# Performance work log

Measured on AMD Instinct MI355X. Metric: run time of the kernel, lower is better.

Reference implementation:

```python
import jax, jax.numpy as jnp
import numpy as np


def setup_inputs() -> dict:
    key = jax.random.key(0)
    k_x, k_q, k_k, k_v = jax.random.split(key, 4)
    seq_len, d_in, d_out = 4096, 1024, 1024
    x = jax.random.normal(k_x, (seq_len, d_in), dtype=jnp.float32)
    # torch nn.Linear weights are [d_out, d_in]; applied as x @ W.T
    scale = 1.0 / np.sqrt(d_in)
    Wq = jax.random.uniform(k_q, (d_out, d_in), jnp.float32, -scale, scale)
    Wk = jax.random.uniform(k_k, (d_out, d_in), jnp.float32, -scale, scale)
    Wv = jax.random.uniform(k_v, (d_out, d_in), jnp.float32, -scale, scale)
    return {"x": x, "Wq": Wq, "Wk": Wk, "Wv": Wv}


def reference(x, Wq, Wk, Wv):
    # x: [S, d_in]; Wq/Wk/Wv: [d_out, d_in]
    queries = x @ Wq.T          # [S, d_out]
    keys = x @ Wk.T             # [S, d_out]
    values = x @ Wv.T           # [S, d_out]
    d_k = keys.shape[-1]
    attn_scores = queries @ keys.T                      # [S, S]
    attn_weights = jax.nn.softmax(attn_scores / jnp.sqrt(jnp.float32(d_k)), axis=-1)
    S = attn_scores.shape[0]
    tril = jnp.tril(jnp.ones((S, S), dtype=attn_weights.dtype))
    masked = tril * attn_weights
    masked_norm = masked / jnp.sum(masked, axis=-1, keepdims=True)
    context_vec = masked_norm @ values                  # [S, d_out]
    return context_vec
```

## Files before the change

### kernel.cpp

```cpp
#include <hip/hip_runtime.h>
#include <hip/hip_bf16.h>


typedef __bf16 bf16_t;
typedef __bf16 bf16x4v __attribute__((ext_vector_type(4)));
typedef __bf16 bf16x8 __attribute__((ext_vector_type(8)));
typedef float f32x4 __attribute__((ext_vector_type(4)));
typedef unsigned char u8;
typedef long long i64_t;

#define AS1 __attribute__((address_space(1)))
#define AS3 __attribute__((address_space(3)))
#define WAIT_VMCNT(N) asm volatile("s_waitcnt vmcnt(" #N ")" ::: "memory")
#define BARRIER_RAW() asm volatile("s_barrier" ::: "memory")

__device__ __forceinline__ void async_copy16(const void* g, void* l) {
    __builtin_amdgcn_global_load_lds((AS1 void*)(g), (AS3 void*)(l), 16, 0, 0);
}

__device__ __forceinline__ u8 f32_to_fp8(float v) {
    return (u8)(__builtin_amdgcn_cvt_pk_fp8_f32(v, v, 0, false) & 0xff);
}

__device__ __forceinline__ void store_conv(float* p, float v) { *p = v; }
__device__ __forceinline__ void store_conv(bf16_t* p, float v) { *p = (bf16_t)v; }
__device__ __forceinline__ void store_conv(u8* p, float v) { *p = f32_to_fp8(v); }

__device__ __forceinline__ float sum32(const float* p) {
    const f32x4* v = (const f32x4*)p;
    float s = 0.f;
#pragma unroll
    for (int u = 0; u < 8; ++u) {
        f32x4 a = v[u];
        s += a[0] + a[1] + a[2] + a[3];
    }
    return s;
}

template <int EPI, typename OutT>
__device__ __forceinline__ void gemm_tile_bf16(const bf16_t* __restrict__ A, int lda,
                                               const bf16_t* __restrict__ B, int ldb,
                                               OutT* __restrict__ C, int ldc,
                                               int kb0, int kb1, float alpha,
                                               char* __restrict__ smem,
                                               const float* __restrict__ inv) {
    constexpr int BK = 64;
    bf16_t* As = (bf16_t*)smem;
    bf16_t* Bs = (bf16_t*)(smem + 32768);
    const int tid = threadIdx.x;
    const int lane = tid & 63, wave = tid >> 6;
    const int wm = wave >> 1, wn = wave & 1;
    const int q = lane >> 4, l16 = lane & 15;

    f32x4 acc[4][4] = {};

    const bf16_t* aSrc[4];
    const bf16_t* bSrc[4];
    int ldsOff[4];
#pragma unroll
    for (int it = 0; it < 4; ++it) {
        int c = it * 256 + tid;
        int r = c >> 3, b = c & 7;
        int sb = b ^ (r & 7);
        aSrc[it] = A + (size_t)r * lda + sb * 8;
        bSrc[it] = B + (size_t)r * ldb + sb * 8;
        ldsOff[it] = c * 8;
    }

    {
        const int k0 = kb0 * BK;
#pragma unroll
        for (int it = 0; it < 4; ++it) async_copy16(aSrc[it] + k0, &As[ldsOff[it]]);
#pragma unroll
        for (int it = 0; it < 4; ++it) async_copy16(bSrc[it] + k0, &Bs[ldsOff[it]]);
    }

    int cur = 0;
    for (int kb = kb0; kb < kb1; ++kb) {
        if (kb + 1 < kb1) {
            const int k0 = (kb + 1) * BK;
            const int boff = (cur ^ 1) * 8192;
#pragma unroll
            for (int it = 0; it < 4; ++it) async_copy16(aSrc[it] + k0, &As[boff + ldsOff[it]]);
#pragma unroll
            for (int it = 0; it < 4; ++it) async_copy16(bSrc[it] + k0, &Bs[boff + ldsOff[it]]);
            WAIT_VMCNT(8);
        } else {
            WAIT_VMCNT(0);
        }
        __builtin_amdgcn_sched_barrier(0);
        BARRIER_RAW();
        const bf16_t* Ab = As + cur * 8192;
        const bf16_t* Bb = Bs + cur * 8192;
        __builtin_amdgcn_s_setprio(1);
#pragma unroll
        for (int k2 = 0; k2 < 2; ++k2) {
            bf16x8 af[4], bfr[4];
#pragma unroll
            for (int mt = 0; mt < 4; ++mt) {
                int m = wm * 64 + mt * 16 + l16;
                int blk = (k2 * 4 + q) ^ (m & 7);
                af[mt] = *(const bf16x8*)&Ab[m * BK + blk * 8];
            }
#pragma unroll
            for (int nt = 0; nt < 4; ++nt) {
                int nn = wn * 64 + nt * 16 + l16;
                int blk = (k2 * 4 + q) ^ (nn & 7);
                bfr[nt] = *(const bf16x8*)&Bb[nn * BK + blk * 8];
            }
#pragma unroll
            for (int mt = 0; mt < 4; ++mt)
#pragma unroll
                for (int nt = 0; nt < 4; ++nt)
                    acc[mt][nt] = __builtin_amdgcn_mfma_f32_16x16x32_bf16(
                        af[mt], bfr[nt], acc[mt][nt], 0, 0, 0);
        }
        __builtin_amdgcn_s_setprio(0);
        BARRIER_RAW();
        cur ^= 1;
    }

    constexpr int S = (int)sizeof(OutT);
    constexpr int RB = 128 * S;
    const int row0 = wm * 64, col0 = wn * 64;
#pragma unroll
    for (int mt = 0; mt < 4; ++mt)
#pragma unroll
        for (int nt = 0; nt < 4; ++nt)
#pragma unroll
            for (int r = 0; r < 4; ++r) {
                int lr = row0 + mt * 16 + q * 4 + r;
                int lc = col0 + nt * 16 + l16;
                float v = acc[mt][nt][r];
                v = (EPI == 2) ? v * inv[lr] : v * alpha;
                int cb = (lc * S) >> 4;
                int sw = cb ^ ((lr >> 2) & 7);
                store_conv((OutT*)(smem + lr * RB + (sw << 4) + ((lc * S) & 15)), v);
            }
    __syncthreads();
#pragma unroll
    for (int p = 0; p < 4 * S; ++p) {
        int g = p * 4096 + tid * 16;
        int r = g / RB;
        int wb = g & (RB - 1);
        int sc = (wb >> 4) ^ ((r >> 2) & 7);
        f32x4 val = *(const f32x4*)(smem + r * RB + (sc << 4));
        *(f32x4*)((char*)C + (size_t)r * ((size_t)ldc * S) + wb) = val;
    }
}

__device__ __forceinline__ void scores_tile_fp8(const u8* __restrict__ A, int lda,
                                                const u8* __restrict__ B, int ldb,
                                                bf16_t* __restrict__ C, int ldc,
                                                float alpha, char* __restrict__ smem,
                                                float* __restrict__ partial,
                                                int gr0, int gc0) {
    u8* As = (u8*)smem;
    u8* Bs = (u8*)(smem + 32768);
    const int tid = threadIdx.x;
    const int lane = tid & 63, wave = tid >> 6;
    const int wm = wave >> 1, wn = wave & 1;
    const int q = lane >> 4, l16 = lane & 15;

    f32x4 acc[4][4] = {};

    const u8* aSrc[4];
    const u8* bSrc[4];
    int ldsOff[4];
#pragma unroll
    for (int it = 0; it < 4; ++it) {
        int c = it * 256 + tid;
        int r = c >> 3, b = c & 7;
        int sb = b ^ (r & 7);
        aSrc[it] = A + (size_t)r * lda + sb * 16;
        bSrc[it] = B + (size_t)r * ldb + sb * 16;
        ldsOff[it] = c * 16;
    }

    {
#pragma unroll
        for (int it = 0; it < 4; ++it) async_copy16(aSrc[it], &As[ldsOff[it]]);
#pragma unroll
        for (int it = 0; it < 4; ++it) async_copy16(bSrc[it], &Bs[ldsOff[it]]);
    }

    int cur = 0;
    for (int kb = 0; kb < 8; ++kb) {
        if (kb < 7) {
            const int k0 = (kb + 1) * 128;
            const int boff = (cur ^ 1) * 16384;
#pragma unroll
            for (int it = 0; it < 4; ++it) async_copy16(aSrc[it] + k0, &As[boff + ldsOff[it]]);
#pragma unroll
            for (int it = 0; it < 4; ++it) async_copy16(bSrc[it] + k0, &Bs[boff + ldsOff[it]]);
            WAIT_VMCNT(8);
        } else {
            WAIT_VMCNT(0);
        }
        __builtin_amdgcn_sched_barrier(0);
        BARRIER_RAW();
        const u8* Ab = As + cur * 16384;
        const u8* Bb = Bs + cur * 16384;
        __builtin_amdgcn_s_setprio(1);
#pragma unroll
        for (int k2 = 0; k2 < 4; ++k2) {
            i64_t af[4], bfr[4];
            const int cb = 2 * k2 + (q >> 1), co = (q & 1) * 8;
#pragma unroll
            for (int mt = 0; mt < 4; ++mt) {
                int m = wm * 64 + mt * 16 + l16;
                af[mt] = *(const i64_t*)&Ab[m * 128 + ((cb ^ (m & 7)) << 4) + co];
            }
#pragma unroll
            for (int nt = 0; nt < 4; ++nt) {
                int nn = wn * 64 + nt * 16 + l16;
                bfr[nt] = *(const i64_t*)&Bb[nn * 128 + ((cb ^ (nn & 7)) << 4) + co];
            }
#pragma unroll
            for (int mt = 0; mt < 4; ++mt)
#pragma unroll
                for (int nt = 0; nt < 4; ++nt)
                    acc[mt][nt] = __builtin_amdgcn_mfma_f32_16x16x32_fp8_fp8(
                        af[mt], bfr[nt], acc[mt][nt], 0, 0, 0);
        }
        __builtin_amdgcn_s_setprio(0);
        BARRIER_RAW();
        cur ^= 1;
    }

    float* sred = (float*)(smem + 32768);
    const int row0 = wm * 64, col0 = wn * 64;
    float esum[4][4];
#pragma unroll
    for (int mt = 0; mt < 4; ++mt)
#pragma unroll
        for (int r = 0; r < 4; ++r) esum[mt][r] = 0.f;
#pragma unroll
    for (int mt = 0; mt < 4; ++mt)
#pragma unroll
        for (int nt = 0; nt < 4; ++nt)
#pragma unroll
            for (int r = 0; r < 4; ++r) {
                int lr = row0 + mt * 16 + q * 4 + r;
                int lc = col0 + nt * 16 + l16;
                float pe = (gc0 + lc > gr0 + lr) ? 0.f : __expf(acc[mt][nt][r] * alpha);
                esum[mt][r] += pe;
                int sw = (lc >> 3) ^ ((lr >> 2) & 7);
                *(bf16_t*)(smem + lr * 256 + (sw << 4) + ((lc * 2) & 15)) = (bf16_t)pe;
            }
#pragma unroll
    for (int mt = 0; mt < 4; ++mt)
#pragma unroll
        for (int r = 0; r < 4; ++r) {
#pragma unroll
            for (int off = 1; off < 16; off <<= 1)
                esum[mt][r] += __shfl_xor(esum[mt][r], off, 64);
            if (l16 == 0) sred[(row0 + mt * 16 + q * 4 + r) * 2 + wn] = esum[mt][r];
        }
    __syncthreads();
#pragma unroll
    for (int p = 0; p < 8; ++p) {
        int g = p * 4096 + tid * 16;
        int r = g >> 8;
        int wb = g & 255;
        int sc = (wb >> 4) ^ ((r >> 2) & 7);
        f32x4 val = *(const f32x4*)(smem + r * 256 + (sc << 4));
        *(f32x4*)((char*)C + (size_t)r * ((size_t)ldc * 2) + wb) = val;
    }
    if (tid < 128) partial[(size_t)tid * 32] = sred[tid * 2] + sred[tid * 2 + 1];
}

__global__ __launch_bounds__(256) void k_qkv(const bf16_t* __restrict__ xb,
                                             const bf16_t* __restrict__ wqk,
                                             u8* __restrict__ qk) {
    __shared__ __attribute__((aligned(16))) char smem[65536];
    int b = blockIdx.x;
    int bm = b & 31, bn = b >> 5;
    gemm_tile_bf16<0, u8>(xb + (size_t)bm * 128 * 1024, 1024,
                          wqk + (size_t)bn * 128 * 1024, 1024,
                          qk + (size_t)bm * 128 * 2048 + bn * 128, 2048,
                          0, 16, 1.f, smem, nullptr);
}

__global__ __launch_bounds__(256) void k_sv(const bf16_t* __restrict__ xb,
                                            const bf16_t* __restrict__ wvb,
                                            const u8* __restrict__ qk,
                                            bf16_t* __restrict__ vt,
                                            bf16_t* __restrict__ P,
                                            float* __restrict__ rowsum_part) {
    __shared__ __attribute__((aligned(16))) char smem[65536];
    int b = blockIdx.x;
    if (b < 256) {
        int bm = b & 7, bn = b >> 3;
        gemm_tile_bf16<0, bf16_t>(wvb + (size_t)bm * 128 * 1024, 1024,
                                  xb + (size_t)bn * 128 * 1024, 1024,
                                  vt + (size_t)bm * 128 * 4096 + bn * 128, 4096,
                                  0, 16, 1.f, smem, nullptr);
        return;
    }
    int t = b - 256;
    int bm = (int)((sqrtf(8.f * (float)t + 1.f) - 1.f) * 0.5f);
    while (bm * (bm + 1) / 2 > t) --bm;
    while ((bm + 1) * (bm + 2) / 2 <= t) ++bm;
    int bn = t - bm * (bm + 1) / 2;
    scores_tile_fp8(qk + (size_t)bm * 128 * 2048, 2048,
                    qk + 1024 + (size_t)bn * 128 * 2048, 2048,
                    P + (size_t)bm * 128 * 4096 + bn * 128, 4096,
                    0.03125f, smem,
                    rowsum_part + (size_t)bm * 128 * 32 + bn,
                    bm * 128, bn * 128);
    if (bn == bm) {
        float* rp = rowsum_part + (size_t)bm * 128 * 32;
        int tid = threadIdx.x;
        for (int r = tid >> 4; r < 128; r += 16)
            for (int u = bm + 1 + (tid & 15); u < 32; u += 16)
                rp[r * 32 + u] = 0.f;
    }
}

__global__ __launch_bounds__(256) void k_pv(const bf16_t* __restrict__ P,
                                            const bf16_t* __restrict__ vt,
                                            const float* __restrict__ rowsum_part,
                                            float* __restrict__ out,
                                            float* __restrict__ partials) {
    __shared__ __attribute__((aligned(16))) char smem[65536];
    __shared__ float sInv[128];
    int b = blockIdx.x;
    int bn = b & 7, g = b >> 3;
    int bm, s, ns;
    if (g < 8)       { bm = g;                 s = 0;            ns = 1; }
    else if (g < 24) { bm = 8 + (g - 8) / 2;   s = (g - 8) % 2;  ns = 2; }
    else if (g < 48) { bm = 16 + (g - 24) / 3; s = (g - 24) % 3; ns = 3; }
    else             { bm = 24 + (g - 48) / 4; s = (g - 48) % 4; ns = 4; }
    int nk = 2 * (bm + 1);
    int kb0 = s * nk / ns;
    int kb1 = (s + 1) * nk / ns;

    const bf16_t* A = P + (size_t)bm * 128 * 4096;
    const bf16_t* B = vt + (size_t)bn * 128 * 4096;
    if (ns == 1) {
        int tid = threadIdx.x;
        if (tid < 128)
            sInv[tid] = 1.f / sum32(rowsum_part + (size_t)(bm * 128 + tid) * 32);
        gemm_tile_bf16<2, float>(A, 4096, B, 4096,
                                 out + (size_t)bm * 128 * 1024 + bn * 128, 1024,
                                 kb0, kb1, 1.f, smem, sInv);
    } else {
        int cum = (bm < 16) ? (bm - 8) * 2
                : (bm < 24) ? 16 + (bm - 16) * 3
                            : 40 + (bm - 24) * 4;
        gemm_tile_bf16<0, float>(A, 4096, B, 4096,
                                 partials + ((size_t)(cum + s) * 8 + bn) * 16384, 128,
                                 kb0, kb1, 1.f, smem, nullptr);
    }
}

__global__ __launch_bounds__(256) void k_reduce(const float* __restrict__ partials,
                                                const float* __restrict__ rowsum_part,
                                                float* __restrict__ out) {
    int b = blockIdx.x;
    int t = b % 192, p = b / 192;
    int bm = t % 24 + 8, bn = t / 24;
    int ns = (bm < 16) ? 2 : (bm < 24) ? 3 : 4;
    int cum = (bm < 16) ? (bm - 8) * 2
            : (bm < 24) ? 16 + (bm - 16) * 3
                        : 40 + (bm - 24) * 4;
    __shared__ float sInv[8];
    int tid = threadIdx.x;
    if (tid < 8) {
        int row = bm * 128 + p * 8 + tid;
        sInv[tid] = 1.f / sum32(rowsum_part + (size_t)row * 32);
    }
    __syncthreads();

    int idx = p * 1024 + tid * 4;
    int lr = idx >> 7, lc = idx & 127;
    float sx = 0.f, sy = 0.f, sz = 0.f, sw = 0.f;
    for (int u = 0; u < ns; ++u) {
        const float4 v = *(const float4*)(partials + ((size_t)(cum + u) * 8 + bn) * 16384 + idx);
        sx += v.x; sy += v.y; sz += v.z; sw += v.w;
    }
    float inv = sInv[lr - p * 8];
    float4 o = {sx * inv, sy * inv, sz * inv, sw * inv};
    *(float4*)(out + (size_t)(bm * 128 + lr) * 1024 + bn * 128 + lc) = o;
}

__global__ __launch_bounds__(256) void cast_to_bf16(const float* __restrict__ x,
                                                    const float* __restrict__ Wq,
                                                    const float* __restrict__ Wk,
                                                    const float* __restrict__ Wv,
                                                    bf16_t* __restrict__ xb,
                                                    bf16_t* __restrict__ wqk,
                                                    bf16_t* __restrict__ wv) {
    const int NX = (4096 * 1024) / 4;
    const int NW = (1024 * 1024) / 4;
    int idx = blockIdx.x * 256 + threadIdx.x;
    const float* src;
    bf16_t* dst;
    int off;
    if (idx < NX) {
        src = x; dst = xb; off = idx;
    } else if (idx < NX + NW) {
        src = Wq; dst = wqk; off = idx - NX;
    } else if (idx < NX + 2 * NW) {
        src = Wk; dst = wqk + (size_t)NW * 4; off = idx - NX - NW;
    } else {
        src = Wv; dst = wv; off = idx - NX - 2 * NW;
    }
    float4 f = ((const float4*)src)[off];
    bf16x4v o;
    o.x = (bf16_t)f.x; o.y = (bf16_t)f.y; o.z = (bf16_t)f.z; o.w = (bf16_t)f.w;
    *(bf16x4v*)(dst + (size_t)off * 4) = o;
}

extern "C" void kernel_launch(void* const* d_in, const int* in_sizes, int n_in,
                              void* d_out, int out_size, void* d_ws, size_t ws_size,
                              hipStream_t stream) {
    (void)in_sizes; (void)n_in; (void)out_size; (void)ws_size;
    const float* x  = (const float*)d_in[0];
    const float* Wq = (const float*)d_in[1];
    const float* Wk = (const float*)d_in[2];
    const float* Wv = (const float*)d_in[3];
    float* out = (float*)d_out;

    char* ws = (char*)d_ws;
    bf16_t* xb   = (bf16_t*)(ws + (size_t)0);
    bf16_t* wqk  = (bf16_t*)(ws + ((size_t)8 << 20));
    bf16_t* wvb  = (bf16_t*)(ws + ((size_t)12 << 20));
    u8*     qk   = (u8*)(ws + ((size_t)14 << 20));
    bf16_t* vt   = (bf16_t*)(ws + ((size_t)22 << 20));
    bf16_t* P    = (bf16_t*)(ws + ((size_t)30 << 20));
    float* rowsp = (float*)(ws + ((size_t)62 << 20));
    float* parts = (float*)(ws + ((size_t)64 << 20));

    cast_to_bf16<<<7168, 256, 0, stream>>>(x, Wq, Wk, Wv, xb, wqk, wvb);

    k_qkv<<<512, 256, 0, stream>>>(xb, wqk, qk);

    k_sv<<<784, 256, 0, stream>>>(xb, wvb, qk, vt, P, rowsp);

    k_pv<<<640, 256, 0, stream>>>(P, vt, rowsp, out, parts);
    k_reduce<<<3072, 256, 0, stream>>>(parts, rowsp, out);
}
```

Measured before the change: 181.2 us.

## Split scores into dedicated 256x128 fp8 kernel and merge V projection into QK GEMM

Moves the V-projection GEMM out of the scores launch and into the QK projection launch, so Q/K/V projections run as one 768-block grid. The causal score tiles get their own kernel with 512-thread blocks, 256x128 tiles and 96KB shared memory. It uses a restructured double-buffered loop that interleaves fragment reads, async prefetch and MFMA phases. Larger tiles raise operand reuse per LDS load but give fewer blocks (272) and one block per CU, which may hurt load balance on the triangular work.

```diff
diff --git a/kernel.cpp b/kernel.cpp
--- a/kernel.cpp
+++ b/kernel.cpp
@@ -149,172 +149,225 @@
     }
 }
 
-__device__ __forceinline__ void scores_tile_fp8(const u8* __restrict__ A, int lda,
-                                                const u8* __restrict__ B, int ldb,
-                                                bf16_t* __restrict__ C, int ldc,
-                                                float alpha, char* __restrict__ smem,
-                                                float* __restrict__ partial,
-                                                int gr0, int gc0) {
-    u8* As = (u8*)smem;
-    u8* Bs = (u8*)(smem + 32768);
+__device__ __forceinline__ void read_afrags(i64_t af[4][2], const u8* Ab,
+                                            int wm, int mh, int k2h,
+                                            int l16, int q) {
+#pragma unroll
+    for (int mt = 0; mt < 4; ++mt)
+#pragma unroll
+        for (int kk = 0; kk < 2; ++kk) {
+            int m = wm * 128 + (mh * 4 + mt) * 16 + l16;
+            int k2 = k2h * 2 + kk;
+            int cb = 2 * k2 + (q >> 1), co = (q & 1) * 8;
+            af[mt][kk] = *(const i64_t*)&Ab[m * 128 + ((cb ^ (m & 7)) << 4) + co];
+        }
+}
+__device__ __forceinline__ void read_bfrags(i64_t bf[2][2], const u8* Bb,
+                                            int wn, int k2h, int l16, int q) {
+#pragma unroll
+    for (int nt = 0; nt < 2; ++nt)
+#pragma unroll
+        for (int kk = 0; kk < 2; ++kk) {
+            int nn = wn * 32 + nt * 16 + l16;
+            int k2 = k2h * 2 + kk;
+            int cb = 2 * k2 + (q >> 1), co = (q & 1) * 8;
+            bf[nt][kk] = *(const i64_t*)&Bb[nn * 128 + ((cb ^ (nn & 7)) << 4) + co];
+        }
+}
+
+__global__ __launch_bounds__(512, 1) void k_scores(const u8* __restrict__ qk,
+                                                   bf16_t* __restrict__ P,
+                                                   float* __restrict__ rowsum_part) {
+    __shared__ __attribute__((aligned(16))) char smem[98304];
+    int t = blockIdx.x;
+    int bm = (int)(sqrtf((float)t + 0.25f) - 0.5f);
+    while (bm * (bm + 1) > t) --bm;
+    while ((bm + 1) * (bm + 2) <= t) ++bm;
+    int bn = t - bm * (bm + 1);
+    const u8* A = qk + (size_t)bm * 256 * 2048;
+    const u8* B = qk + 1024 + (size_t)bn * 128 * 2048;
+    const int gr0 = bm * 256, gc0 = bn * 128;
+    bf16_t* Cc = P + (size_t)bm * 256 * 4096 + bn * 128;
+    float* partial = rowsum_part + (size_t)bm * 256 * 32 + bn;
+
     const int tid = threadIdx.x;
     const int lane = tid & 63, wave = tid >> 6;
-    const int wm = wave >> 1, wn = wave & 1;
+    const int wm = wave >> 2, wn = wave & 3;
     const int q = lane >> 4, l16 = lane & 15;
 
-    f32x4 acc[4][4] = {};
-
-    const u8* aSrc[4];
-    const u8* bSrc[4];
-    int ldsOff[4];
-#pragma unroll
-    for (int it = 0; it < 4; ++it) {
-        int c = it * 256 + tid;
-        int r = c >> 3, b = c & 7;
-        int sb = b ^ (r & 7);
-        aSrc[it] = A + (size_t)r * lda + sb * 16;
-        bSrc[it] = B + (size_t)r * ldb + sb * 16;
-        ldsOff[it] = c * 16;
-    }
-
-    {
-#pragma unroll
-        for (int it = 0; it < 4; ++it) async_copy16(aSrc[it], &As[ldsOff[it]]);
-#pragma unroll
-        for (int it = 0; it < 4; ++it) async_copy16(bSrc[it], &Bs[ldsOff[it]]);
-    }
-
-    int cur = 0;
-    for (int kb = 0; kb < 8; ++kb) {
-        if (kb < 7) {
-            const int k0 = (kb + 1) * 128;
-            const int boff = (cur ^ 1) * 16384;
-#pragma unroll
-            for (int it = 0; it < 4; ++it) async_copy16(aSrc[it] + k0, &As[boff + ldsOff[it]]);
-#pragma unroll
-            for (int it = 0; it < 4; ++it) async_copy16(bSrc[it] + k0, &Bs[boff + ldsOff[it]]);
-            WAIT_VMCNT(8);
-        } else {
-            WAIT_VMCNT(0);
-        }
-        __builtin_amdgcn_sched_barrier(0);
-        BARRIER_RAW();
-        const u8* Ab = As + cur * 16384;
-        const u8* Bb = Bs + cur * 16384;
+    f32x4 acc[8][2] = {};
+
+    const u8* aSrc[4]; int aOff[4];
+    const u8* bSrc[2]; int bOff[2];
+#pragma unroll
+    for (int pp = 0; pp < 4; ++pp) {
+        int g16 = pp * 512 + tid, r = g16 >> 3, b = g16 & 7, sb = b ^ (r & 7);
+        aSrc[pp] = A + (size_t)r * 2048 + sb * 16;
+        aOff[pp] = g16 * 16;
+    }
+#pragma unroll
+    for (int pp = 0; pp < 2; ++pp) {
+        int g16 = pp * 512 + tid, r = g16 >> 3, b = g16 & 7, sb = b ^ (r & 7);
+        bSrc[pp] = B + (size_t)r * 2048 + sb * 16;
+        bOff[pp] = g16 * 16;
+    }
+
+#pragma unroll
+    for (int pp = 0; pp < 4; ++pp) async_copy16(aSrc[pp], smem + aOff[pp]);
+#pragma unroll
+    for (int pp = 0; pp < 2; ++pp) async_copy16(bSrc[pp], smem + 32768 + bOff[pp]);
+    WAIT_VMCNT(0);
+    BARRIER_RAW();
+
+    for (int kt = 0; kt < 8; ++kt) {
+        const char* bufb = smem + (kt & 1) * 49152;
+        char* bufn = smem + ((kt & 1) ^ 1) * 49152;
+        const u8* Ab = (const u8*)bufb;
+        const u8* Bb = (const u8*)(bufb + 32768);
+        const int k0n = (kt + 1) * 128;
+        i64_t af[4][2], bf[2][2];
+
+        read_afrags(af, Ab, wm, 0, 0, l16, q);
+        read_bfrags(bf, Bb, wn, 0, l16, q);
+        if (kt < 7) {
+            async_copy16(aSrc[0] + k0n, bufn + aOff[0]);
+            async_copy16(aSrc[1] + k0n, bufn + aOff[1]);
+            async_copy16(bSrc[0] + k0n, bufn + 32768 + bOff[0]);
+        }
+        BARRIER_RAW();
         __builtin_amdgcn_s_setprio(1);
 #pragma unroll
-        for (int k2 = 0; k2 < 4; ++k2) {
-            i64_t af[4], bfr[4];
-            const int cb = 2 * k2 + (q >> 1), co = (q & 1) * 8;
-#pragma unroll
-            for (int mt = 0; mt < 4; ++mt) {
-                int m = wm * 64 + mt * 16 + l16;
-                af[mt] = *(const i64_t*)&Ab[m * 128 + ((cb ^ (m & 7)) << 4) + co];
-            }
-#pragma unroll
-            for (int nt = 0; nt < 4; ++nt) {
-                int nn = wn * 64 + nt * 16 + l16;
-                bfr[nt] = *(const i64_t*)&Bb[nn * 128 + ((cb ^ (nn & 7)) << 4) + co];
-            }
-#pragma unroll
-            for (int mt = 0; mt < 4; ++mt)
-#pragma unroll
-                for (int nt = 0; nt < 4; ++nt)
+        for (int mt = 0; mt < 4; ++mt)
+#pragma unroll
+            for (int nt = 0; nt < 2; ++nt)
+#pragma unroll
+                for (int kk = 0; kk < 2; ++kk)
                     acc[mt][nt] = __builtin_amdgcn_mfma_f32_16x16x32_fp8_fp8(
-                        af[mt], bfr[nt], acc[mt][nt], 0, 0, 0);
-        }
+                        af[mt][kk], bf[nt][kk], acc[mt][nt], 0, 0, 0);
         __builtin_amdgcn_s_setprio(0);
         BARRIER_RAW();
-        cur ^= 1;
-    }
-
-    float* sred = (float*)(smem + 32768);
-    const int row0 = wm * 64, col0 = wn * 64;
-    float esum[4][4];
-#pragma unroll
-    for (int mt = 0; mt < 4; ++mt)
+
+        read_afrags(af, Ab, wm, 1, 0, l16, q);
+        if (kt < 7) {
+            async_copy16(aSrc[2] + k0n, bufn + aOff[2]);
+            async_copy16(aSrc[3] + k0n, bufn + aOff[3]);
+            async_copy16(bSrc[1] + k0n, bufn + 32768 + bOff[1]);
+        }
+        BARRIER_RAW();
+        __builtin_amdgcn_s_setprio(1);
+#pragma unroll
+        for (int mt = 0; mt < 4; ++mt)
+#pragma unroll
+            for (int nt = 0; nt < 2; ++nt)
+#pragma unroll
+                for (int kk = 0; kk < 2; ++kk)
+                    acc[4 + mt][nt] = __builtin_amdgcn_mfma_f32_16x16x32_fp8_fp8(
+                        af[mt][kk], bf[nt][kk], acc[4 + mt][nt], 0, 0, 0);
+        __builtin_amdgcn_s_setprio(0);
+        BARRIER_RAW();
+
+        read_afrags(af, Ab, wm, 0, 1, l16, q);
+        read_bfrags(bf, Bb, wn, 1, l16, q);
+        BARRIER_RAW();
+        __builtin_amdgcn_s_setprio(1);
+#pragma unroll
+        for (int mt = 0; mt < 4; ++mt)
+#pragma unroll
+            for (int nt = 0; nt < 2; ++nt)
+#pragma unroll
+                for (int kk = 0; kk < 2; ++kk)
+                    acc[mt][nt] = __builtin_amdgcn_mfma_f32_16x16x32_fp8_fp8(
+                        af[mt][kk], bf[nt][kk], acc[mt][nt], 0, 0, 0);
+        __builtin_amdgcn_s_setprio(0);
+        BARRIER_RAW();
+
+        read_afrags(af, Ab, wm, 1, 1, l16, q);
+        BARRIER_RAW();
+        __builtin_amdgcn_s_setprio(1);
+#pragma unroll
+        for (int mt = 0; mt < 4; ++mt)
+#pragma unroll
+            for (int nt = 0; nt < 2; ++nt)
+#pragma unroll
+                for (int kk = 0; kk < 2; ++kk)
+                    acc[4 + mt][nt] = __builtin_amdgcn_mfma_f32_16x16x32_fp8_fp8(
+                        af[mt][kk], bf[nt][kk], acc[4 + mt][nt], 0, 0, 0);
+        __builtin_amdgcn_s_setprio(0);
+        if (kt < 7) WAIT_VMCNT(0);
+        BARRIER_RAW();
+    }
+
+    float* sred = (float*)(smem + 65536);
+    float esum[8][4];
+#pragma unroll
+    for (int mt = 0; mt < 8; ++mt)
 #pragma unroll
         for (int r = 0; r < 4; ++r) esum[mt][r] = 0.f;
 #pragma unroll
-    for (int mt = 0; mt < 4; ++mt)
-#pragma unroll
-        for (int nt = 0; nt < 4; ++nt)
+    for (int mt = 0; mt < 8; ++mt)
+#pragma unroll
+        for (int nt = 0; nt < 2; ++nt)
 #pragma unroll
             for (int r = 0; r < 4; ++r) {
-                int lr = row0 + mt * 16 + q * 4 + r;
-                int lc = col0 + nt * 16 + l16;
-                float pe = (gc0 + lc > gr0 + lr) ? 0.f : __expf(acc[mt][nt][r] * alpha);
+                int lr = wm * 128 + mt * 16 + q * 4 + r;
+                int lc = wn * 32 + nt * 16 + l16;
+                float pe = (gc0 + lc > gr0 + lr) ? 0.f
+                                                 : __expf(acc[mt][nt][r] * 0.03125f);
                 esum[mt][r] += pe;
                 int sw = (lc >> 3) ^ ((lr >> 2) & 7);
                 *(bf16_t*)(smem + lr * 256 + (sw << 4) + ((lc * 2) & 15)) = (bf16_t)pe;
             }
 #pragma unroll
-    for (int mt = 0; mt < 4; ++mt)
+    for (int mt = 0; mt < 8; ++mt)
 #pragma unroll
         for (int r = 0; r < 4; ++r) {
+            float s = esum[mt][r];
 #pragma unroll
             for (int off = 1; off < 16; off <<= 1)
-                esum[mt][r] += __shfl_xor(esum[mt][r], off, 64);
-            if (l16 == 0) sred[(row0 + mt * 16 + q * 4 + r) * 2 + wn] = esum[mt][r];
+                s += __shfl_xor(s, off, 64);
+            if (l16 == 0)
+                sred[(wm * 128 + mt * 16 + q * 4 + r) * 4 + wn] = s;
         }
     __syncthreads();
 #pragma unroll
     for (int p = 0; p < 8; ++p) {
-        int g = p * 4096 + tid * 16;
-        int r = g >> 8;
-        int wb = g & 255;
+        int g = p * 8192 + tid * 16;
+        int r = g >> 8, wb = g & 255;
         int sc = (wb >> 4) ^ ((r >> 2) & 7);
         f32x4 val = *(const f32x4*)(smem + r * 256 + (sc << 4));
-        *(f32x4*)((char*)C + (size_t)r * ((size_t)ldc * 2) + wb) = val;
-    }
-    if (tid < 128) partial[(size_t)tid * 32] = sred[tid * 2] + sred[tid * 2 + 1];
-}
-
-__global__ __launch_bounds__(256) void k_qkv(const bf16_t* __restrict__ xb,
-                                             const bf16_t* __restrict__ wqk,
-                                             u8* __restrict__ qk) {
+        *(f32x4*)((char*)Cc + (size_t)r * 8192 + wb) = val;
+    }
+    if (tid < 256)
+        partial[(size_t)tid * 32] =
+            sred[tid * 4] + sred[tid * 4 + 1] + sred[tid * 4 + 2] + sred[tid * 4 + 3];
+    if (bn == 2 * bm + 1) {
+        float* rp = rowsum_part + (size_t)bm * 256 * 32;
+        for (int r = tid >> 4; r < 256; r += 32)
+            for (int u = 2 * bm + 2 + (tid & 15); u < 32; u += 16)
+                rp[r * 32 + u] = 0.f;
+    }
+}
+
+__global__ __launch_bounds__(256) void k_qkvv(const bf16_t* __restrict__ xb,
+                                              const bf16_t* __restrict__ wqk,
+                                              const bf16_t* __restrict__ wvb,
+                                              u8* __restrict__ qk,
+                                              bf16_t* __restrict__ vt) {
     __shared__ __attribute__((aligned(16))) char smem[65536];
     int b = blockIdx.x;
-    int bm = b & 31, bn = b >> 5;
-    gemm_tile_bf16<0, u8>(xb + (size_t)bm * 128 * 1024, 1024,
-                          wqk + (size_t)bn * 128 * 1024, 1024,
-                          qk + (size_t)bm * 128 * 2048 + bn * 128, 2048,
-                          0, 16, 1.f, smem, nullptr);
-}
-
-__global__ __launch_bounds__(256) void k_sv(const bf16_t* __restrict__ xb,
-                                            const bf16_t* __restrict__ wvb,
-                                            const u8* __restrict__ qk,
-                                            bf16_t* __restrict__ vt,
-                                            bf16_t* __restrict__ P,
-                                            float* __restrict__ rowsum_part) {
-    __shared__ __attribute__((aligned(16))) char smem[65536];
-    int b = blockIdx.x;
-    if (b < 256) {
-        int bm = b & 7, bn = b >> 3;
+    if (b < 512) {
+        int bm = b & 31, bn = b >> 5;
+        gemm_tile_bf16<0, u8>(xb + (size_t)bm * 128 * 1024, 1024,
+                              wqk + (size_t)bn * 128 * 1024, 1024,
+                              qk + (size_t)bm * 128 * 2048 + bn * 128, 2048,
+                              0, 16, 1.f, smem, nullptr);
+    } else {
+        int bb = b - 512;
+        int bm = bb & 7, bn = bb >> 3;
         gemm_tile_bf16<0, bf16_t>(wvb + (size_t)bm * 128 * 1024, 1024,
                                   xb + (size_t)bn * 128 * 1024, 1024,
                                   vt + (size_t)bm * 128 * 4096 + bn * 128, 4096,
                                   0, 16, 1.f, smem, nullptr);
-        return;
-    }
-    int t = b - 256;
-    int bm = (int)((sqrtf(8.f * (float)t + 1.f) - 1.f) * 0.5f);
-    while (bm * (bm + 1) / 2 > t) --bm;
-    while ((bm + 1) * (bm + 2) / 2 <= t) ++bm;
-    int bn = t - bm * (bm + 1) / 2;
-    scores_tile_fp8(qk + (size_t)bm * 128 * 2048, 2048,
-                    qk + 1024 + (size_t)bn * 128 * 2048, 2048,
-                    P + (size_t)bm * 128 * 4096 + bn * 128, 4096,
-                    0.03125f, smem,
-                    rowsum_part + (size_t)bm * 128 * 32 + bn,
-                    bm * 128, bn * 128);
-    if (bn == bm) {
-        float* rp = rowsum_part + (size_t)bm * 128 * 32;
-        int tid = threadIdx.x;
-        for (int r = tid >> 4; r < 128; r += 16)
-            for (int u = bm + 1 + (tid & 15); u < 32; u += 16)
-                rp[r * 32 + u] = 0.f;
     }
 }
 
@@ -435,9 +488,9 @@
 
     cast_to_bf16<<<7168, 256, 0, stream>>>(x, Wq, Wk, Wv, xb, wqk, wvb);
 
-    k_qkv<<<512, 256, 0, stream>>>(xb, wqk, qk);
-
-    k_sv<<<784, 256, 0, stream>>>(xb, wvb, qk, vt, P, rowsp);
+    k_qkvv<<<768, 256, 0, stream>>>(xb, wqk, wvb, qk, vt);
+
+    k_scores<<<272, 512, 0, stream>>>(qk, P, rowsp);
 
     k_pv<<<640, 256, 0, stream>>>(P, vt, rowsp, out, parts);
     k_reduce<<<3072, 256, 0, stream>>>(parts, rowsp, out);
```

Measured after the change: 206.8 us. 14.2% more time.

## Restructure fp8 scores GEMM into 4-stage 64-wide K pipeline with ping-pong phases

Applied to the files above, without the earlier changes.

Replaces the double-buffered 128-wide K loop in the fp8 scores tile with a four-slot ring of 64-wide K chunks, prefetching three chunks ahead. Each K step is split into two phases (top and bottom M halves), with the A and B loads for the next slot interleaved between barriers. The aim is to hide global-to-LDS latency better and overlap LDS reads with MFMA work. It adds more barriers per K step and uses a new LDS swizzle.

```diff
diff --git a/kernel.cpp b/kernel.cpp
--- a/kernel.cpp
+++ b/kernel.cpp
@@ -12,6 +12,7 @@
 #define AS1 __attribute__((address_space(1)))
 #define AS3 __attribute__((address_space(3)))
 #define WAIT_VMCNT(N) asm volatile("s_waitcnt vmcnt(" #N ")" ::: "memory")
+#define WAIT_LGKM0() asm volatile("s_waitcnt lgkmcnt(0)" ::: "memory")
 #define BARRIER_RAW() asm volatile("s_barrier" ::: "memory")
 
 __device__ __forceinline__ void async_copy16(const void* g, void* l) {
@@ -155,8 +156,6 @@
                                                 float alpha, char* __restrict__ smem,
                                                 float* __restrict__ partial,
                                                 int gr0, int gc0) {
-    u8* As = (u8*)smem;
-    u8* Bs = (u8*)(smem + 32768);
     const int tid = threadIdx.x;
     const int lane = tid & 63, wave = tid >> 6;
     const int wm = wave >> 1, wn = wave & 1;
@@ -164,68 +163,102 @@
 
     f32x4 acc[4][4] = {};
 
-    const u8* aSrc[4];
-    const u8* bSrc[4];
-    int ldsOff[4];
-#pragma unroll
-    for (int it = 0; it < 4; ++it) {
-        int c = it * 256 + tid;
-        int r = c >> 3, b = c & 7;
-        int sb = b ^ (r & 7);
-        aSrc[it] = A + (size_t)r * lda + sb * 16;
-        bSrc[it] = B + (size_t)r * ldb + sb * 16;
-        ldsOff[it] = c * 16;
-    }
-
-    {
-#pragma unroll
-        for (int it = 0; it < 4; ++it) async_copy16(aSrc[it], &As[ldsOff[it]]);
-#pragma unroll
-        for (int it = 0; it < 4; ++it) async_copy16(bSrc[it], &Bs[ldsOff[it]]);
-    }
-
-    int cur = 0;
-    for (int kb = 0; kb < 8; ++kb) {
-        if (kb < 7) {
-            const int k0 = (kb + 1) * 128;
-            const int boff = (cur ^ 1) * 16384;
-#pragma unroll
-            for (int it = 0; it < 4; ++it) async_copy16(aSrc[it] + k0, &As[boff + ldsOff[it]]);
-#pragma unroll
-            for (int it = 0; it < 4; ++it) async_copy16(bSrc[it] + k0, &Bs[boff + ldsOff[it]]);
-            WAIT_VMCNT(8);
-        } else {
-            WAIT_VMCNT(0);
+    const u8* aS[2];
+    const u8* bS[2];
+    int lOff[2];
+#pragma unroll
+    for (int p = 0; p < 2; ++p) {
+        int g = p * 256 + tid, r = g >> 2, c = g & 3;
+        int sc = c ^ ((r >> 1) & 3);
+        aS[p] = A + (size_t)r * lda + sc * 16;
+        bS[p] = B + (size_t)r * ldb + sc * 16;
+        lOff[p] = g * 16;
+    }
+
+#pragma unroll
+    for (int h = 0; h < 3; ++h) {
+        char* s = smem + h * 16384;
+        async_copy16(aS[0] + h * 64, s + lOff[0]);
+        async_copy16(aS[1] + h * 64, s + lOff[1]);
+        async_copy16(bS[0] + h * 64, s + 8192 + lOff[0]);
+        async_copy16(bS[1] + h * 64, s + 8192 + lOff[1]);
+    }
+    WAIT_VMCNT(8);
+    __builtin_amdgcn_sched_barrier(0);
+    BARRIER_RAW();
+
+    for (int h = 0; h < 16; ++h) {
+        const u8* Ab = (const u8*)(smem + (h & 3) * 16384);
+        const u8* Bb = Ab + 8192;
+        char* nslot = smem + ((h + 3) & 3) * 16384;
+        const int kn = (h + 3) * 64;
+        i64_t bf[4][2], af[2][2], af2[2][2];
+
+#pragma unroll
+        for (int nt = 0; nt < 4; ++nt)
+#pragma unroll
+            for (int kk = 0; kk < 2; ++kk) {
+                int nn = wn * 64 + nt * 16 + l16;
+                int cb = kk * 2 + (q >> 1);
+                bf[nt][kk] = *(const i64_t*)&Bb[nn * 64 + ((cb ^ ((nn >> 1) & 3)) << 4) + (q & 1) * 8];
+            }
+#pragma unroll
+        for (int mt = 0; mt < 2; ++mt)
+#pragma unroll
+            for (int kk = 0; kk < 2; ++kk) {
+                int m = wm * 64 + mt * 16 + l16;
+                int cb = kk * 2 + (q >> 1);
+                af[mt][kk] = *(const i64_t*)&Ab[m * 64 + ((cb ^ ((m >> 1) & 3)) << 4) + (q & 1) * 8];
+            }
+        if (h <= 12) {
+            async_copy16(aS[0] + kn, nslot + lOff[0]);
+            async_copy16(aS[1] + kn, nslot + lOff[1]);
         }
+        BARRIER_RAW();
+        WAIT_LGKM0();
         __builtin_amdgcn_sched_barrier(0);
-        BARRIER_RAW();
-        const u8* Ab = As + cur * 16384;
-        const u8* Bb = Bs + cur * 16384;
         __builtin_amdgcn_s_setprio(1);
 #pragma unroll
-        for (int k2 = 0; k2 < 4; ++k2) {
-            i64_t af[4], bfr[4];
-            const int cb = 2 * k2 + (q >> 1), co = (q & 1) * 8;
-#pragma unroll
-            for (int mt = 0; mt < 4; ++mt) {
-                int m = wm * 64 + mt * 16 + l16;
-                af[mt] = *(const i64_t*)&Ab[m * 128 + ((cb ^ (m & 7)) << 4) + co];
-            }
-#pragma unroll
-            for (int nt = 0; nt < 4; ++nt) {
-                int nn = wn * 64 + nt * 16 + l16;
-                bfr[nt] = *(const i64_t*)&Bb[nn * 128 + ((cb ^ (nn & 7)) << 4) + co];
-            }
-#pragma unroll
-            for (int mt = 0; mt < 4; ++mt)
-#pragma unroll
-                for (int nt = 0; nt < 4; ++nt)
+        for (int mt = 0; mt < 2; ++mt)
+#pragma unroll
+            for (int nt = 0; nt < 4; ++nt)
+#pragma unroll
+                for (int kk = 0; kk < 2; ++kk)
                     acc[mt][nt] = __builtin_amdgcn_mfma_f32_16x16x32_fp8_fp8(
-                        af[mt], bfr[nt], acc[mt][nt], 0, 0, 0);
+                        af[mt][kk], bf[nt][kk], acc[mt][nt], 0, 0, 0);
+        __builtin_amdgcn_s_setprio(0);
+        BARRIER_RAW();
+
+#pragma unroll
+        for (int mt = 0; mt < 2; ++mt)
+#pragma unroll
+            for (int kk = 0; kk < 2; ++kk) {
+                int m = wm * 64 + (2 + mt) * 16 + l16;
+                int cb = kk * 2 + (q >> 1);
+                af2[mt][kk] = *(const i64_t*)&Ab[m * 64 + ((cb ^ ((m >> 1) & 3)) << 4) + (q & 1) * 8];
+            }
+        if (h <= 12) {
+            async_copy16(bS[0] + kn, nslot + 8192 + lOff[0]);
+            async_copy16(bS[1] + kn, nslot + 8192 + lOff[1]);
         }
+        BARRIER_RAW();
+        WAIT_LGKM0();
+        __builtin_amdgcn_sched_barrier(0);
+        __builtin_amdgcn_s_setprio(1);
+#pragma unroll
+        for (int mt = 0; mt < 2; ++mt)
+#pragma unroll
+            for (int nt = 0; nt < 4; ++nt)
+#pragma unroll
+                for (int kk = 0; kk < 2; ++kk)
+                    acc[2 + mt][nt] = __builtin_amdgcn_mfma_f32_16x16x32_fp8_fp8(
+                        af2[mt][kk], bf[nt][kk], acc[2 + mt][nt], 0, 0, 0);
         __builtin_amdgcn_s_setprio(0);
-        BARRIER_RAW();
-        cur ^= 1;
+        if (h <= 12)      { WAIT_VMCNT(8); }
+        else if (h == 13) { WAIT_VMCNT(4); }
+        else if (h == 14) { WAIT_VMCNT(0); }
+        __builtin_amdgcn_sched_barrier(0);
+        BARRIER_RAW();
     }
 
     float* sred = (float*)(smem + 32768);
```

After: 186.6 us. 3.0% more time.
